# Kernel tuning notes

Measured on AMD Instinct MI355X. Metric: run time of the kernel, lower is better.

## Reference

```python
import jax, jax.numpy as jnp
import numpy as np

N = 100000   # nodes
E = 3200000  # edges
M = 4096     # moves
K = 16       # orders per move
NEG_SLOPE = 0.2  # PyG GATv2Conv default negative_slope

PARAM_SHAPES = {
    'g1_Wl': (10, 15), 'g1_Wr': (10, 15), 'g1_att': (10,), 'g1_b': (10,),
    'g2_Wl': (10, 25), 'g2_Wr': (10, 25), 'g2_att': (10,), 'g2_b': (10,),
    'g3_Wl': (10, 25), 'g3_Wr': (10, 25), 'g3_att': (10,), 'g3_b': (10,),
    'vt_W': (20, 29), 'vt_b': (20,), 'va_W': (1, 20), 'va_b': (1,),
    'vv_W': (10, 20), 'vv_b': (10,), 'vl_W': (1, 10), 'vl_b': (1,),
    'at_W': (20, 48), 'at_b': (20,), 'dt_W': (20, 23), 'dt_b': (20,),
    'oa_W': (1, 20), 'oa_b': (1,), 'ov_W': (1, 20), 'ov_b': (1,),
}
PARAM_NAMES = list(PARAM_SHAPES.keys())


def _linear(x, W, b):
    return x @ W.T + b


def _gatv2(x, src, dst, Wl, Wr, att, b):
    # GATv2Conv (heads=1, self-loops appended by caller), eval mode (no dropout)
    xl = x @ Wl.T  # messages from source nodes
    xr = x @ Wr.T
    e = (jax.nn.leaky_relu(xl[src] + xr[dst], NEG_SLOPE) * att).sum(-1)  # [E+N]
    emax = jax.ops.segment_max(e, dst, num_segments=N)
    ee = jnp.exp(e - emax[dst])
    denom = jax.ops.segment_sum(ee, dst, num_segments=N)
    alpha = ee / denom[dst]
    return jax.ops.segment_sum(alpha[:, None] * xl[src], dst, num_segments=N) + b


def _forward(x1, x2, edges, move_src, move_dst, move_armies, is_attack, params):
    (g1_Wl, g1_Wr, g1_att, g1_b,
     g2_Wl, g2_Wr, g2_att, g2_b,
     g3_Wl, g3_Wr, g3_att, g3_b,
     vt_W, vt_b, va_W, va_b, vv_W, vv_b, vl_W, vl_b,
     at_W, at_b, dt_W, dt_b, oa_W, oa_b, ov_W, ov_b) = params
    x2t = jnp.tile(x2, (N, 1))  # [N,4]
    self_idx = jnp.arange(N, dtype=edges.dtype)
    src = jnp.concatenate([edges[0], self_idx])
    dst = jnp.concatenate([edges[1], self_idx])
    x = jax.nn.relu(_gatv2(x1, src, dst, g1_Wl, g1_Wr, g1_att, g1_b))
    x = jax.nn.relu(_gatv2(jnp.concatenate([x, x1], 1), src, dst, g2_Wl, g2_Wr, g2_att, g2_b))
    x = jax.nn.relu(_gatv2(jnp.concatenate([x, x1], 1), src, dst, g3_Wl, g3_Wr, g3_att, g3_b))  # [N,10]
    # per-move order tensors (vectorized over [M,K]); deploy uses move_src as target
    xs, xd = x[move_src], x[move_dst]       # [M,K,10]
    x1s, x1d = x1[move_src], x1[move_dst]   # [M,K,15]
    extra = 0.6 * move_armies - 0.7 * (x1d[..., 3] + x1d[..., 4])
    attack_in = jnp.concatenate([xs, xd, x1s[..., 3:], x1d[..., 1:],
                                 move_armies[..., None], extra[..., None]], -1)  # [M,K,48]
    deploy_in = jnp.concatenate([xs, x1s[..., 3:], move_armies[..., None]], -1)  # [M,K,23]
    feat = jnp.where(is_attack[..., None] == 1,
                     _linear(attack_in, at_W, at_b),
                     _linear(deploy_in, dt_W, dt_b))
    feat = jax.nn.relu(feat)  # dropout = identity (eval)
    attn = jax.nn.softmax(_linear(feat, oa_W, oa_b), axis=1)  # softmax over orders
    p = (attn * _linear(feat, ov_W, ov_b)).sum(axis=(1, 2))   # [M]
    # value head: attention pooling over all nodes
    Vn = jax.nn.relu(_linear(jnp.concatenate([x, x1, x2t], 1), vt_W, vt_b))  # [N,20]
    vatt = jax.nn.softmax(_linear(Vn, va_W, va_b), axis=0)
    Vp = jax.nn.relu((vatt * _linear(Vn, vv_W, vv_b)).sum(axis=0))
    V = jnp.tanh(_linear(Vp, vl_W, vl_b))[0]
    return V, jax.nn.log_softmax(p, axis=0)


def setup_inputs() -> dict:
    key = jax.random.key(0)
    ks = iter(jax.random.split(key, 64))
    inp = {
        'x1': jax.random.normal(next(ks), (N, 15), jnp.float32),
        'x2': jax.random.normal(next(ks), (4,), jnp.float32),
        'edges': jax.random.randint(next(ks), (2, E), 0, N, jnp.int32),
        'move_src': jax.random.randint(next(ks), (M, K), 0, N, jnp.int32),
        'move_dst': jax.random.randint(next(ks), (M, K), 0, N, jnp.int32),
        'move_armies': jax.random.uniform(next(ks), (M, K), jnp.float32) * 10.0,
        'is_attack': jax.random.randint(next(ks), (M, K), 0, 2, jnp.int32),
    }
    for name, shape in PARAM_SHAPES.items():
        inp[name] = jax.random.normal(next(ks), shape, jnp.float32) * 0.1
    return inp


def reference(x1, x2, edges, move_src, move_dst, move_armies, is_attack,
              g1_Wl, g1_Wr, g1_att, g1_b, g2_Wl, g2_Wr, g2_att, g2_b,
              g3_Wl, g3_Wr, g3_att, g3_b, vt_W, vt_b, va_W, va_b,
              vv_W, vv_b, vl_W, vl_b, at_W, at_b, dt_W, dt_b,
              oa_W, oa_b, ov_W, ov_b):
    params = (g1_Wl, g1_Wr, g1_att, g1_b, g2_Wl, g2_Wr, g2_att, g2_b,
              g3_Wl, g3_Wr, g3_att, g3_b, vt_W, vt_b, va_W, va_b,
              vv_W, vv_b, vl_W, vl_b, at_W, at_b, dt_W, dt_b,
              oa_W, oa_b, ov_W, ov_b)
    return _forward(x1, x2, edges, move_src, move_dst, move_armies, is_attack, params)
```

## Files before the change

kernel.cpp:

```cpp
#include <hip/hip_runtime.h>
#include <hip/hip_bf16.h>
#include <hip/hip_fp16.h>
#include <math.h>

#define NN 100000
#define NE 3200000
#define MM 4096
#define KK 16
#define NEG_SLOPE 0.2f
#define SUB 8
#define BSH 8
#define NB 391
#define PCH 4096
#define FCAP 9728
#define XS 12

__device__ __forceinline__ void load_h10(const __half* __restrict__ base, long node, float* xs) {
    const uint2* p2 = (const uint2*)(base + node * XS);
    uint2 w0 = p2[0];
    uint2 w1 = p2[1];
    unsigned w2 = *(const unsigned*)(base + node * XS + 8);
    float2 f;
    f = __half22float2(*(const __half2*)&w0.x); xs[0] = f.x; xs[1] = f.y;
    f = __half22float2(*(const __half2*)&w0.y); xs[2] = f.x; xs[3] = f.y;
    f = __half22float2(*(const __half2*)&w1.x); xs[4] = f.x; xs[5] = f.y;
    f = __half22float2(*(const __half2*)&w1.y); xs[6] = f.x; xs[7] = f.y;
    f = __half22float2(*(const __half2*)&w2);   xs[8] = f.x; xs[9] = f.y;
}
__device__ __forceinline__ void store_h10(__half* __restrict__ base, long node, const float* v) {
    unsigned u[5];
    #pragma unroll
    for (int q = 0; q < 5; q++) {
        __half2 h = __floats2half2_rn(v[2*q], v[2*q+1]);
        u[q] = *(unsigned*)&h;
    }
    uint2* p2 = (uint2*)(base + node * XS);
    p2[0] = make_uint2(u[0], u[1]);
    p2[1] = make_uint2(u[2], u[3]);
    *(unsigned*)(base + node * XS + 8) = u[4];
}

__global__ __launch_bounds__(512) void partition_kernel(const int* __restrict__ edges,
                                                        int* __restrict__ cnt,
                                                        unsigned* __restrict__ recs) {
    __shared__ unsigned rl[PCH];
    __shared__ unsigned srt[PCH];
    __shared__ unsigned short bb[PCH];
    __shared__ unsigned short bbs[PCH];
    __shared__ int h[NB];
    __shared__ int sc[512];
    __shared__ int lb[NB];
    __shared__ int gb[NB];
    __shared__ int cur[NB];
    const int total = NE + NN;
    int base = blockIdx.x * PCH;
    int n = min(PCH, total - base);
    int t = threadIdx.x;
    for (int i = t; i < NB; i += 512) { h[i] = 0; cur[i] = 0; }
    __syncthreads();
    for (int j = t; j < n; j += 512) {
        int i = base + j;
        int s, d;
        if (i < NE) { s = edges[i]; d = edges[NE + i]; }
        else        { s = i - NE; d = s; }
        rl[j] = ((unsigned)(d & 255) << 17) | (unsigned)s;
        int b = d >> BSH;
        bb[j] = (unsigned short)b;
        atomicAdd(&h[b], 1);
    }
    __syncthreads();
    int hv = (t < NB) ? h[t] : 0;
    sc[t] = hv;
    __syncthreads();
    for (int off = 1; off < 512; off <<= 1) {
        int v = (t >= off) ? sc[t - off] : 0;
        __syncthreads();
        sc[t] += v;
        __syncthreads();
    }
    if (t < NB) {
        lb[t] = sc[t] - hv;
        if (hv > 0) gb[t] = atomicAdd(&cnt[t], hv);
    }
    __syncthreads();
    for (int j = t; j < n; j += 512) {
        int b = bb[j];
        int l = atomicAdd(&cur[b], 1);
        int dst = lb[b] + l;
        srt[dst] = rl[j];
        bbs[dst] = (unsigned short)b;
    }
    __syncthreads();
    for (int j = t; j < n; j += 512) {
        int b = bbs[j];
        int pos = gb[b] + (j - lb[b]);
        if (pos < FCAP) recs[(long)b * FCAP + pos] = srt[j];
    }
}

__global__ void bucket_scan_kernel(const int* __restrict__ cnt, int* __restrict__ bbase) {
    __shared__ int part[512];
    int t = threadIdx.x;
    int c = (t < NB) ? min(cnt[t], FCAP) : 0;
    part[t] = c;
    __syncthreads();
    for (int off = 1; off < 512; off <<= 1) {
        int v = (t >= off) ? part[t - off] : 0;
        __syncthreads();
        part[t] += v;
        __syncthreads();
    }
    if (t < NB) bbase[t] = part[t] - c;
    if (t == NB - 1) bbase[NB] = part[t];
}

__global__ __launch_bounds__(1024) void fine_sort_kernel(const unsigned* __restrict__ recs,
                                                         const int* __restrict__ cnt,
                                                         const int* __restrict__ bbase,
                                                         int* __restrict__ csr_src,
                                                         int* __restrict__ offsets) {
    __shared__ unsigned rl[FCAP];
    __shared__ int hist[256];
    __shared__ int sc[256];
    __shared__ int hb[257];
    __shared__ int cur[256];
    int b = blockIdx.x;
    int beg = bbase[b];
    int nb = min(cnt[b], FCAP);
    int t = threadIdx.x;
    int nodebase = b << BSH;
    int nnodes = min(256, NN - nodebase);
    if (t < 256) { hist[t] = 0; cur[t] = 0; }
    __syncthreads();
    const unsigned* rsrc = recs + (long)b * FCAP;
    for (int j = t; j < nb; j += 1024) {
        unsigned r = rsrc[j];
        rl[j] = r;
        atomicAdd(&hist[r >> 17], 1);
    }
    __syncthreads();
    int hv = (t < 256) ? hist[t] : 0;
    if (t < 256) sc[t] = hv;
    __syncthreads();
    for (int off = 1; off < 256; off <<= 1) {
        int v = 0;
        if (t < 256 && t >= off) v = sc[t - off];
        __syncthreads();
        if (t < 256) sc[t] += v;
        __syncthreads();
    }
    if (t < 256) hb[t] = sc[t] - hv;
    if (t == 0) hb[256] = nb;
    __syncthreads();
    for (int j = t; j < nb; j += 1024) {
        unsigned r = rl[j];
        int l = r >> 17;
        int p = hb[l] + atomicAdd(&cur[l], 1);
        csr_src[beg + p] = (int)(r & 0x1FFFFu);
    }
    if (t < nnodes) offsets[nodebase + t] = beg + hb[t];
    if (b == NB - 1 && t == 0) offsets[NN] = beg + nb;
}

__global__ void linear1_kernel(const float* __restrict__ x1,
                               const float* __restrict__ Wl,
                               const float* __restrict__ Wr,
                               __half* __restrict__ xlh,
                               float* __restrict__ xr) {
    int i = blockIdx.x * blockDim.x + threadIdx.x;
    if (i >= NN) return;
    float in[15];
    #pragma unroll
    for (int j = 0; j < 15; j++) in[j] = x1[i * 15 + j];
    float sl[10];
    #pragma unroll
    for (int o = 0; o < 10; o++) {
        float l = 0.f, r = 0.f;
        #pragma unroll
        for (int j = 0; j < 15; j++) {
            l += Wl[o * 15 + j] * in[j];
            r += Wr[o * 15 + j] * in[j];
        }
        sl[o] = l;
        xr[(long)i * XS + o] = r;
    }
    store_h10(xlh, i, sl);
}

template<bool FUSE_NEXT>
__global__ void gat_aggregate_kernel(const int* __restrict__ csr_src,
                                     const int* __restrict__ offsets,
                                     const __half* __restrict__ xlh,
                                     const float* __restrict__ xr,
                                     const float* __restrict__ att,
                                     const float* __restrict__ b,
                                     const float* __restrict__ x1,
                                     const float* __restrict__ nWl,
                                     const float* __restrict__ nWr,
                                     __half* __restrict__ xlo,
                                     float* __restrict__ xro,
                                     float* __restrict__ xout)
{
    int t = blockIdx.x * blockDim.x + threadIdx.x;
    int node = t / SUB;
    int lane = t % SUB;
    if (node >= NN) return;
    float xrn[12], a[10];
    const float4* xr4 = (const float4*)(xr + (long)node * XS);
    #pragma unroll
    for (int q = 0; q < 3; q++) {
        float4 v = xr4[q];
        xrn[4*q] = v.x; xrn[4*q+1] = v.y; xrn[4*q+2] = v.z; xrn[4*q+3] = v.w;
    }
    #pragma unroll
    for (int h = 0; h < 10; h++) a[h] = att[h];
    int beg = offsets[node], end = offsets[node + 1];
    float den = 0.f, num[10];
    #pragma unroll
    for (int h = 0; h < 10; h++) num[h] = 0.f;
    for (int j = beg + lane; j < end; j += SUB) {
        int s = csr_src[j];
        float xs[10];
        load_h10(xlh, s, xs);
        float e = 0.f;
        #pragma unroll
        for (int h = 0; h < 10; h++) {
            float v = xs[h] + xrn[h];
            v = (v >= 0.f) ? v : NEG_SLOPE * v;
            e += v * a[h];
        }
        float w = __expf(e);
        den += w;
        #pragma unroll
        for (int h = 0; h < 10; h++) num[h] += w * xs[h];
    }
    #pragma unroll
    for (int off = SUB / 2; off; off >>= 1) {
        den += __shfl_xor(den, off, SUB);
        #pragma unroll
        for (int h = 0; h < 10; h++) num[h] += __shfl_xor(num[h], off, SUB);
    }
    float inv = 1.f / den;
    float xo[10];
    #pragma unroll
    for (int h = 0; h < 10; h++) xo[h] = fmaxf(num[h] * inv + b[h], 0.f);
    if (FUSE_NEXT) {
        if (lane < 5) {
            float in2[25];
            #pragma unroll
            for (int h = 0; h < 10; h++) in2[h] = xo[h];
            #pragma unroll
            for (int h = 0; h < 15; h++) in2[10 + h] = x1[(long)node * 15 + h];
            int o0 = 2 * lane, o1 = 2 * lane + 1;
            float sl0 = 0.f, sl1 = 0.f, sr0 = 0.f, sr1 = 0.f;
            #pragma unroll
            for (int j = 0; j < 25; j++) {
                sl0 += nWl[o0 * 25 + j] * in2[j];
                sl1 += nWl[o1 * 25 + j] * in2[j];
                sr0 += nWr[o0 * 25 + j] * in2[j];
                sr1 += nWr[o1 * 25 + j] * in2[j];
            }
            __half2 hp = __floats2half2_rn(sl0, sl1);
            *(unsigned*)(xlo + (long)node * XS + o0) = *(unsigned*)&hp;
            *(float2*)(xro + (long)node * XS + o0) = make_float2(sr0, sr1);
        }
    } else {
        if (lane == 0) {
            #pragma unroll
            for (int h = 0; h < 10; h++) xout[(long)node * XS + h] = xo[h];
        }
    }
}

__global__ void move_kernel(const float* __restrict__ x,
                            const float* __restrict__ x1,
                            const int* __restrict__ msrc,
                            const int* __restrict__ mdst,
                            const float* __restrict__ armies,
                            const int* __restrict__ isatk,
                            const float* __restrict__ at_W, const float* __restrict__ at_b,
                            const float* __restrict__ dt_W, const float* __restrict__ dt_b,
                            const float* __restrict__ oa_W, const float* __restrict__ oa_b,
                            const float* __restrict__ ov_W, const float* __restrict__ ov_b,
                            float* __restrict__ p) {
    int t = blockIdx.x * blockDim.x + threadIdx.x;
    int m = t >> 4;
    int k = t & 15;
    int s = msrc[t], d = mdst[t];
    float arm = armies[t];
    bool atk = (isatk[t] == 1);
    float xsrc[12];
    const float4* xs4 = (const float4*)(x + (long)s * XS);
    #pragma unroll
    for (int q = 0; q < 3; q++) {
        float4 v = xs4[q];
        xsrc[4*q] = v.x; xsrc[4*q+1] = v.y; xsrc[4*q+2] = v.z; xsrc[4*q+3] = v.w;
    }
    float feat[20];
    if (atk) {
        float in[48];
        #pragma unroll
        for (int h = 0; h < 10; h++) in[h] = xsrc[h];
        const float4* xd4 = (const float4*)(x + (long)d * XS);
        float xdst[12];
        #pragma unroll
        for (int q = 0; q < 3; q++) {
            float4 v = xd4[q];
            xdst[4*q] = v.x; xdst[4*q+1] = v.y; xdst[4*q+2] = v.z; xdst[4*q+3] = v.w;
        }
        #pragma unroll
        for (int h = 0; h < 10; h++) in[10 + h] = xdst[h];
        #pragma unroll
        for (int h = 0; h < 12; h++) in[20 + h] = x1[(long)s * 15 + 3 + h];
        #pragma unroll
        for (int h = 0; h < 14; h++) in[32 + h] = x1[(long)d * 15 + 1 + h];
        in[46] = arm;
        in[47] = 0.6f * arm - 0.7f * (x1[(long)d * 15 + 3] + x1[(long)d * 15 + 4]);
        #pragma unroll
        for (int o = 0; o < 20; o++) {
            float sum = at_b[o];
            #pragma unroll
            for (int j = 0; j < 48; j++) sum += at_W[o * 48 + j] * in[j];
            feat[o] = fmaxf(sum, 0.f);
        }
    } else {
        float in[23];
        #pragma unroll
        for (int h = 0; h < 10; h++) in[h] = xsrc[h];
        #pragma unroll
        for (int h = 0; h < 12; h++) in[10 + h] = x1[(long)s * 15 + 3 + h];
        in[22] = arm;
        #pragma unroll
        for (int o = 0; o < 20; o++) {
            float sum = dt_b[o];
            #pragma unroll
            for (int j = 0; j < 23; j++) sum += dt_W[o * 23 + j] * in[j];
            feat[o] = fmaxf(sum, 0.f);
        }
    }
    float oa = oa_b[0], ov = ov_b[0];
    #pragma unroll
    for (int j = 0; j < 20; j++) {
        oa += oa_W[j] * feat[j];
        ov += ov_W[j] * feat[j];
    }
    float mx = oa;
    #pragma unroll
    for (int off = 8; off; off >>= 1) mx = fmaxf(mx, __shfl_xor(mx, off, 16));
    float w = __expf(oa - mx);
    float nume = w * ov;
    float den = w;
    #pragma unroll
    for (int off = 8; off; off >>= 1) {
        nume += __shfl_xor(nume, off, 16);
        den  += __shfl_xor(den,  off, 16);
    }
    if (k == 0) p[m] = nume / den;
}

__global__ void logsoftmax_kernel(const float* __restrict__ p, float* __restrict__ out) {
    __shared__ float sm[256];
    int tid = threadIdx.x;
    float mx = -INFINITY;
    for (int i = tid; i < MM; i += 256) mx = fmaxf(mx, p[i]);
    sm[tid] = mx; __syncthreads();
    for (int s = 128; s; s >>= 1) { if (tid < s) sm[tid] = fmaxf(sm[tid], sm[tid + s]); __syncthreads(); }
    mx = sm[0]; __syncthreads();
    float sum = 0.f;
    for (int i = tid; i < MM; i += 256) sum += expf(p[i] - mx);
    sm[tid] = sum; __syncthreads();
    for (int s = 128; s; s >>= 1) { if (tid < s) sm[tid] += sm[tid + s]; __syncthreads(); }
    float ls = mx + logf(sm[0]);
    for (int i = tid; i < MM; i += 256) out[i] = p[i] - ls;
}

__global__ void value12_kernel(const float* __restrict__ x,
                               const float* __restrict__ x1,
                               const float* __restrict__ x2,
                               const float* __restrict__ vt_W, const float* __restrict__ vt_b,
                               const float* __restrict__ va_W, const float* __restrict__ va_b,
                               const float* __restrict__ vv_W, const float* __restrict__ vv_b,
                               float* __restrict__ partials) {
    __shared__ float sm[4][11];
    int i = blockIdx.x * blockDim.x + threadIdx.x;
    float w = 0.f;
    float acc[10];
    #pragma unroll
    for (int h = 0; h < 10; h++) acc[h] = 0.f;
    if (i < NN) {
        float in[29];
        const float4* xi4 = (const float4*)(x + (long)i * XS);
        float xi[12];
        #pragma unroll
        for (int q = 0; q < 3; q++) {
            float4 v = xi4[q];
            xi[4*q] = v.x; xi[4*q+1] = v.y; xi[4*q+2] = v.z; xi[4*q+3] = v.w;
        }
        #pragma unroll
        for (int h = 0; h < 10; h++) in[h] = xi[h];
        #pragma unroll
        for (int h = 0; h < 15; h++) in[10 + h] = x1[(long)i * 15 + h];
        #pragma unroll
        for (int h = 0; h < 4; h++) in[25 + h] = x2[h];
        float Vn[20];
        #pragma unroll
        for (int o = 0; o < 20; o++) {
            float s = vt_b[o];
            #pragma unroll
            for (int j = 0; j < 29; j++) s += vt_W[o * 29 + j] * in[j];
            Vn[o] = fmaxf(s, 0.f);
        }
        float lg = va_b[0];
        #pragma unroll
        for (int j = 0; j < 20; j++) lg += va_W[j] * Vn[j];
        w = __expf(lg);
        #pragma unroll
        for (int o = 0; o < 10; o++) {
            float s = vv_b[o];
            #pragma unroll
            for (int j = 0; j < 20; j++) s += vv_W[o * 20 + j] * Vn[j];
            acc[o] = w * s;
        }
    }
    #pragma unroll
    for (int off = 32; off; off >>= 1) {
        w += __shfl_xor(w, off, 64);
        #pragma unroll
        for (int h = 0; h < 10; h++) acc[h] += __shfl_xor(acc[h], off, 64);
    }
    int wid = threadIdx.x >> 6;
    if ((threadIdx.x & 63) == 0) {
        #pragma unroll
        for (int h = 0; h < 10; h++) sm[wid][h] = acc[h];
        sm[wid][10] = w;
    }
    __syncthreads();
    if (threadIdx.x < 11) {
        int c = threadIdx.x;
        partials[(long)blockIdx.x * 12 + c] = sm[0][c] + sm[1][c] + sm[2][c] + sm[3][c];
    }
}

__global__ void value3_kernel(const float* __restrict__ partials, int nparts,
                              const float* __restrict__ vl_W, const float* __restrict__ vl_b,
                              float* __restrict__ out0) {
    int lane = threadIdx.x;
    float s[11];
    #pragma unroll
    for (int c = 0; c < 11; c++) s[c] = 0.f;
    for (int j = lane; j < nparts; j += 64)
        #pragma unroll
        for (int c = 0; c < 11; c++) s[c] += partials[(long)j * 12 + c];
    #pragma unroll
    for (int off = 32; off; off >>= 1)
        #pragma unroll
        for (int c = 0; c < 11; c++) s[c] += __shfl_xor(s[c], off, 64);
    if (lane == 0) {
        float inv = 1.0f / s[10];
        float v = vl_b[0];
        #pragma unroll
        for (int h = 0; h < 10; h++) v += vl_W[h] * fmaxf(s[h] * inv, 0.f);
        out0[0] = tanhf(v);
    }
}

extern "C" void kernel_launch(void* const* d_in, const int* in_sizes, int n_in,
                              void* d_out, int out_size, void* d_ws, size_t ws_size,
                              hipStream_t stream) {
    const float* x1      = (const float*)d_in[0];
    const float* x2      = (const float*)d_in[1];
    const int*   edges   = (const int*)d_in[2];
    const int*   msrc    = (const int*)d_in[3];
    const int*   mdst    = (const int*)d_in[4];
    const float* armies  = (const float*)d_in[5];
    const int*   isatk   = (const int*)d_in[6];
    const float* g1_Wl = (const float*)d_in[7],  *g1_Wr = (const float*)d_in[8];
    const float* g1_att= (const float*)d_in[9],  *g1_b  = (const float*)d_in[10];
    const float* g2_Wl = (const float*)d_in[11], *g2_Wr = (const float*)d_in[12];
    const float* g2_att= (const float*)d_in[13], *g2_b  = (const float*)d_in[14];
    const float* g3_Wl = (const float*)d_in[15], *g3_Wr = (const float*)d_in[16];
    const float* g3_att= (const float*)d_in[17], *g3_b  = (const float*)d_in[18];
    const float* vt_W  = (const float*)d_in[19], *vt_b  = (const float*)d_in[20];
    const float* va_W  = (const float*)d_in[21], *va_b  = (const float*)d_in[22];
    const float* vv_W  = (const float*)d_in[23], *vv_b  = (const float*)d_in[24];
    const float* vl_W  = (const float*)d_in[25], *vl_b  = (const float*)d_in[26];
    const float* at_W  = (const float*)d_in[27], *at_b  = (const float*)d_in[28];
    const float* dt_W  = (const float*)d_in[29], *dt_b  = (const float*)d_in[30];
    const float* oa_W  = (const float*)d_in[31], *oa_b  = (const float*)d_in[32];
    const float* ov_W  = (const float*)d_in[33], *ov_b  = (const float*)d_in[34];

    float* out = (float*)d_out;

    float* ws = (float*)d_ws;
    const long XN = (long)NN * XS;
    __half* xlhA = (__half*)ws;
    __half* xlhB = xlhA + XN;
    float* xrA = (float*)(xlhB + XN);
    float* xrB = xrA + XN;
    float* xF  = xrB + XN;
    int* csr_src = (int*)(xF + XN);
    int* offsets = csr_src + (NE + NN);
    unsigned* recs = (unsigned*)(offsets + NN + 4);
    int* cnt   = (int*)(recs + (long)NB * FCAP);
    int* bbase = cnt + NB + 1;
    float* pbuf = (float*)(bbase + NB + 3);
    float* partials = pbuf + MM;

    const int nodeBlocks = (NN + 255) / 256;
    const int aggBlocks  = ((long)NN * SUB + 255) / 256;
    const int partBlocks = (NE + NN + PCH - 1) / PCH;

    hipMemsetAsync(cnt, 0, NB * sizeof(int), stream);
    partition_kernel<<<partBlocks, 512, 0, stream>>>(edges, cnt, recs);
    bucket_scan_kernel<<<1, 512, 0, stream>>>(cnt, bbase);
    fine_sort_kernel<<<NB, 1024, 0, stream>>>(recs, cnt, bbase, csr_src, offsets);

    linear1_kernel<<<nodeBlocks, 256, 0, stream>>>(x1, g1_Wl, g1_Wr, xlhA, xrA);
    gat_aggregate_kernel<true><<<aggBlocks, 256, 0, stream>>>(
        csr_src, offsets, xlhA, xrA, g1_att, g1_b, x1, g2_Wl, g2_Wr, xlhB, xrB, nullptr);
    gat_aggregate_kernel<true><<<aggBlocks, 256, 0, stream>>>(
        csr_src, offsets, xlhB, xrB, g2_att, g2_b, x1, g3_Wl, g3_Wr, xlhA, xrA, nullptr);
    gat_aggregate_kernel<false><<<aggBlocks, 256, 0, stream>>>(
        csr_src, offsets, xlhA, xrA, g3_att, g3_b, x1, nullptr, nullptr, nullptr, nullptr, xF);

    move_kernel<<<(MM * KK) / 256, 256, 0, stream>>>(
        xF, x1, msrc, mdst, armies, isatk,
        at_W, at_b, dt_W, dt_b, oa_W, oa_b, ov_W, ov_b, pbuf);
    logsoftmax_kernel<<<1, 256, 0, stream>>>(pbuf, out + 1);

    value12_kernel<<<nodeBlocks, 256, 0, stream>>>(
        xF, x1, x2, vt_W, vt_b, va_W, va_b, vv_W, vv_b, partials);
    value3_kernel<<<1, 64, 0, stream>>>(partials, nodeBlocks, vl_W, vl_b, out);
}
```

Before: 366.9 us.

## Aggregate directly from coarse bucket records with shared-memory atomics, drop fine sort

Removes the bucket scan and fine CSR sort kernels. Each GAT aggregation block now processes one 256-node destination bucket straight from the partitioned records, accumulating numerators and denominators with shared-memory float atomics. The next layer's linear projection runs from shared weights. The fp16 feature rows are padded to 16 halves so one 16-byte load fetches most of a row, and the partition kernel uses 1024 threads. This saves the sort passes and CSR writes at the cost of heavy shared-atomic contention and only 391 blocks per layer, which may leave the GPU underoccupied.

```diff
diff --git a/kernel.cpp b/kernel.cpp
--- a/kernel.cpp
+++ b/kernel.cpp
@@ -8,47 +8,22 @@
 #define MM 4096
 #define KK 16
 #define NEG_SLOPE 0.2f
-#define SUB 8
 #define BSH 8
 #define NB 391
 #define PCH 4096
 #define FCAP 9728
 #define XS 12
-
-__device__ __forceinline__ void load_h10(const __half* __restrict__ base, long node, float* xs) {
-    const uint2* p2 = (const uint2*)(base + node * XS);
-    uint2 w0 = p2[0];
-    uint2 w1 = p2[1];
-    unsigned w2 = *(const unsigned*)(base + node * XS + 8);
-    float2 f;
-    f = __half22float2(*(const __half2*)&w0.x); xs[0] = f.x; xs[1] = f.y;
-    f = __half22float2(*(const __half2*)&w0.y); xs[2] = f.x; xs[3] = f.y;
-    f = __half22float2(*(const __half2*)&w1.x); xs[4] = f.x; xs[5] = f.y;
-    f = __half22float2(*(const __half2*)&w1.y); xs[6] = f.x; xs[7] = f.y;
-    f = __half22float2(*(const __half2*)&w2);   xs[8] = f.x; xs[9] = f.y;
-}
-__device__ __forceinline__ void store_h10(__half* __restrict__ base, long node, const float* v) {
-    unsigned u[5];
-    #pragma unroll
-    for (int q = 0; q < 5; q++) {
-        __half2 h = __floats2half2_rn(v[2*q], v[2*q+1]);
-        u[q] = *(unsigned*)&h;
-    }
-    uint2* p2 = (uint2*)(base + node * XS);
-    p2[0] = make_uint2(u[0], u[1]);
-    p2[1] = make_uint2(u[2], u[3]);
-    *(unsigned*)(base + node * XS + 8) = u[4];
-}
-
-__global__ __launch_bounds__(512) void partition_kernel(const int* __restrict__ edges,
-                                                        int* __restrict__ cnt,
-                                                        unsigned* __restrict__ recs) {
+#define XSH 16
+
+__global__ __launch_bounds__(1024) void partition_kernel(const int* __restrict__ edges,
+                                                         int* __restrict__ cnt,
+                                                         unsigned* __restrict__ recs) {
     __shared__ unsigned rl[PCH];
     __shared__ unsigned srt[PCH];
     __shared__ unsigned short bb[PCH];
     __shared__ unsigned short bbs[PCH];
     __shared__ int h[NB];
-    __shared__ int sc[512];
+    __shared__ int sc[1024];
     __shared__ int lb[NB];
     __shared__ int gb[NB];
     __shared__ int cur[NB];
@@ -56,9 +31,9 @@
     int base = blockIdx.x * PCH;
     int n = min(PCH, total - base);
     int t = threadIdx.x;
-    for (int i = t; i < NB; i += 512) { h[i] = 0; cur[i] = 0; }
-    __syncthreads();
-    for (int j = t; j < n; j += 512) {
+    if (t < NB) { h[t] = 0; cur[t] = 0; }
+    __syncthreads();
+    for (int j = t; j < n; j += 1024) {
         int i = base + j;
         int s, d;
         if (i < NE) { s = edges[i]; d = edges[NE + i]; }
@@ -72,7 +47,7 @@
     int hv = (t < NB) ? h[t] : 0;
     sc[t] = hv;
     __syncthreads();
-    for (int off = 1; off < 512; off <<= 1) {
+    for (int off = 1; off < 1024; off <<= 1) {
         int v = (t >= off) ? sc[t - off] : 0;
         __syncthreads();
         sc[t] += v;
@@ -83,7 +58,7 @@
         if (hv > 0) gb[t] = atomicAdd(&cnt[t], hv);
     }
     __syncthreads();
-    for (int j = t; j < n; j += 512) {
+    for (int j = t; j < n; j += 1024) {
         int b = bb[j];
         int l = atomicAdd(&cur[b], 1);
         int dst = lb[b] + l;
@@ -91,75 +66,11 @@
         bbs[dst] = (unsigned short)b;
     }
     __syncthreads();
-    for (int j = t; j < n; j += 512) {
+    for (int j = t; j < n; j += 1024) {
         int b = bbs[j];
         int pos = gb[b] + (j - lb[b]);
         if (pos < FCAP) recs[(long)b * FCAP + pos] = srt[j];
     }
-}
-
-__global__ void bucket_scan_kernel(const int* __restrict__ cnt, int* __restrict__ bbase) {
-    __shared__ int part[512];
-    int t = threadIdx.x;
-    int c = (t < NB) ? min(cnt[t], FCAP) : 0;
-    part[t] = c;
-    __syncthreads();
-    for (int off = 1; off < 512; off <<= 1) {
-        int v = (t >= off) ? part[t - off] : 0;
-        __syncthreads();
-        part[t] += v;
-        __syncthreads();
-    }
-    if (t < NB) bbase[t] = part[t] - c;
-    if (t == NB - 1) bbase[NB] = part[t];
-}
-
-__global__ __launch_bounds__(1024) void fine_sort_kernel(const unsigned* __restrict__ recs,
-                                                         const int* __restrict__ cnt,
-                                                         const int* __restrict__ bbase,
-                                                         int* __restrict__ csr_src,
-                                                         int* __restrict__ offsets) {
-    __shared__ unsigned rl[FCAP];
-    __shared__ int hist[256];
-    __shared__ int sc[256];
-    __shared__ int hb[257];
-    __shared__ int cur[256];
-    int b = blockIdx.x;
-    int beg = bbase[b];
-    int nb = min(cnt[b], FCAP);
-    int t = threadIdx.x;
-    int nodebase = b << BSH;
-    int nnodes = min(256, NN - nodebase);
-    if (t < 256) { hist[t] = 0; cur[t] = 0; }
-    __syncthreads();
-    const unsigned* rsrc = recs + (long)b * FCAP;
-    for (int j = t; j < nb; j += 1024) {
-        unsigned r = rsrc[j];
-        rl[j] = r;
-        atomicAdd(&hist[r >> 17], 1);
-    }
-    __syncthreads();
-    int hv = (t < 256) ? hist[t] : 0;
-    if (t < 256) sc[t] = hv;
-    __syncthreads();
-    for (int off = 1; off < 256; off <<= 1) {
-        int v = 0;
-        if (t < 256 && t >= off) v = sc[t - off];
-        __syncthreads();
-        if (t < 256) sc[t] += v;
-        __syncthreads();
-    }
-    if (t < 256) hb[t] = sc[t] - hv;
-    if (t == 0) hb[256] = nb;
-    __syncthreads();
-    for (int j = t; j < nb; j += 1024) {
-        unsigned r = rl[j];
-        int l = r >> 17;
-        int p = hb[l] + atomicAdd(&cur[l], 1);
-        csr_src[beg + p] = (int)(r & 0x1FFFFu);
-    }
-    if (t < nnodes) offsets[nodebase + t] = beg + hb[t];
-    if (b == NB - 1 && t == 0) offsets[NN] = beg + nb;
 }
 
 __global__ void linear1_kernel(const float* __restrict__ x1,
@@ -184,44 +95,72 @@
         sl[o] = l;
         xr[(long)i * XS + o] = r;
     }
-    store_h10(xlh, i, sl);
+    unsigned u[5];
+    #pragma unroll
+    for (int q = 0; q < 5; q++) {
+        __half2 hh = __floats2half2_rn(sl[2*q], sl[2*q+1]);
+        u[q] = *(unsigned*)&hh;
+    }
+    uint4* p4 = (uint4*)(xlh + (long)i * XSH);
+    p4[0] = make_uint4(u[0], u[1], u[2], u[3]);
+    *(unsigned*)(xlh + (long)i * XSH + 8) = u[4];
 }
 
 template<bool FUSE_NEXT>
-__global__ void gat_aggregate_kernel(const int* __restrict__ csr_src,
-                                     const int* __restrict__ offsets,
-                                     const __half* __restrict__ xlh,
-                                     const float* __restrict__ xr,
-                                     const float* __restrict__ att,
-                                     const float* __restrict__ b,
-                                     const float* __restrict__ x1,
-                                     const float* __restrict__ nWl,
-                                     const float* __restrict__ nWr,
-                                     __half* __restrict__ xlo,
-                                     float* __restrict__ xro,
-                                     float* __restrict__ xout)
+__global__ __launch_bounds__(1024) void rec_aggregate_kernel(
+        const unsigned* __restrict__ recs,
+        const int* __restrict__ cnt,
+        const __half* __restrict__ xlh,
+        const float* __restrict__ xr,
+        const float* __restrict__ att,
+        const float* __restrict__ bias,
+        const float* __restrict__ x1,
+        const float* __restrict__ nWl,
+        const float* __restrict__ nWr,
+        __half* __restrict__ xlo,
+        float* __restrict__ xro,
+        float* __restrict__ xout)
 {
-    int t = blockIdx.x * blockDim.x + threadIdx.x;
-    int node = t / SUB;
-    int lane = t % SUB;
-    if (node >= NN) return;
-    float xrn[12], a[10];
-    const float4* xr4 = (const float4*)(xr + (long)node * XS);
-    #pragma unroll
-    for (int q = 0; q < 3; q++) {
-        float4 v = xr4[q];
-        xrn[4*q] = v.x; xrn[4*q+1] = v.y; xrn[4*q+2] = v.z; xrn[4*q+3] = v.w;
-    }
+    __shared__ float xrt[256 * 11];
+    __shared__ float acc[256 * 11];
+    __shared__ float wsh[500];
+    int b = blockIdx.x;
+    int t = threadIdx.x;
+    int nodebase = b << BSH;
+    int nnodes = min(256, NN - nodebase);
+    int nb = min(cnt[b], FCAP);
+    if (t < nnodes) {
+        const float* p = xr + (long)(nodebase + t) * XS;
+        float4 a0 = *(const float4*)p;
+        float4 a1 = *(const float4*)(p + 4);
+        float2 a2 = *(const float2*)(p + 8);
+        float* dst = xrt + t * 11;
+        dst[0]=a0.x; dst[1]=a0.y; dst[2]=a0.z; dst[3]=a0.w;
+        dst[4]=a1.x; dst[5]=a1.y; dst[6]=a1.z; dst[7]=a1.w;
+        dst[8]=a2.x; dst[9]=a2.y;
+    }
+    for (int i = t; i < 256 * 11; i += 1024) acc[i] = 0.f;
+    if (FUSE_NEXT && t < 500) wsh[t] = (t < 250) ? nWl[t] : nWr[t - 250];
+    float a[10];
     #pragma unroll
     for (int h = 0; h < 10; h++) a[h] = att[h];
-    int beg = offsets[node], end = offsets[node + 1];
-    float den = 0.f, num[10];
-    #pragma unroll
-    for (int h = 0; h < 10; h++) num[h] = 0.f;
-    for (int j = beg + lane; j < end; j += SUB) {
-        int s = csr_src[j];
+    __syncthreads();
+    const unsigned* rsrc = recs + (long)b * FCAP;
+    for (int j = t; j < nb; j += 1024) {
+        unsigned r = rsrc[j];
+        int dl = r >> 17;
+        int s = r & 0x1FFFFu;
+        const __half* ph = xlh + (long)s * XSH;
+        uint4 w0 = *(const uint4*)ph;
+        uint2 w1 = *(const uint2*)(ph + 8);
         float xs[10];
-        load_h10(xlh, s, xs);
+        float2 f;
+        f = __half22float2(*(const __half2*)&w0.x); xs[0]=f.x; xs[1]=f.y;
+        f = __half22float2(*(const __half2*)&w0.y); xs[2]=f.x; xs[3]=f.y;
+        f = __half22float2(*(const __half2*)&w0.z); xs[4]=f.x; xs[5]=f.y;
+        f = __half22float2(*(const __half2*)&w0.w); xs[6]=f.x; xs[7]=f.y;
+        f = __half22float2(*(const __half2*)&w1.x); xs[8]=f.x; xs[9]=f.y;
+        const float* xrn = xrt + dl * 11;
         float e = 0.f;
         #pragma unroll
         for (int h = 0; h < 10; h++) {
@@ -230,44 +169,56 @@
             e += v * a[h];
         }
         float w = __expf(e);
-        den += w;
-        #pragma unroll
-        for (int h = 0; h < 10; h++) num[h] += w * xs[h];
-    }
-    #pragma unroll
-    for (int off = SUB / 2; off; off >>= 1) {
-        den += __shfl_xor(den, off, SUB);
-        #pragma unroll
-        for (int h = 0; h < 10; h++) num[h] += __shfl_xor(num[h], off, SUB);
-    }
-    float inv = 1.f / den;
-    float xo[10];
-    #pragma unroll
-    for (int h = 0; h < 10; h++) xo[h] = fmaxf(num[h] * inv + b[h], 0.f);
+        float* pa = acc + dl * 11;
+        #pragma unroll
+        for (int h = 0; h < 10; h++) atomicAdd(&pa[h], w * xs[h]);
+        atomicAdd(&pa[10], w);
+    }
+    __syncthreads();
+    if (t < nnodes) {
+        float* pa = acc + t * 11;
+        float inv = 1.f / pa[10];
+        #pragma unroll
+        for (int h = 0; h < 10; h++)
+            pa[h] = fmaxf(pa[h] * inv + bias[h], 0.f);
+    }
+    __syncthreads();
     if (FUSE_NEXT) {
-        if (lane < 5) {
+        int node = t >> 2;
+        int sub = t & 3;
+        if (node < nnodes) {
             float in2[25];
-            #pragma unroll
-            for (int h = 0; h < 10; h++) in2[h] = xo[h];
-            #pragma unroll
-            for (int h = 0; h < 15; h++) in2[10 + h] = x1[(long)node * 15 + h];
-            int o0 = 2 * lane, o1 = 2 * lane + 1;
-            float sl0 = 0.f, sl1 = 0.f, sr0 = 0.f, sr1 = 0.f;
-            #pragma unroll
-            for (int j = 0; j < 25; j++) {
-                sl0 += nWl[o0 * 25 + j] * in2[j];
-                sl1 += nWl[o1 * 25 + j] * in2[j];
-                sr0 += nWr[o0 * 25 + j] * in2[j];
-                sr1 += nWr[o1 * 25 + j] * in2[j];
+            const float* pa = acc + node * 11;
+            #pragma unroll
+            for (int h = 0; h < 10; h++) in2[h] = pa[h];
+            const float* px1 = x1 + (long)(nodebase + node) * 15;
+            #pragma unroll
+            for (int h = 0; h < 15; h++) in2[10 + h] = px1[h];
+            #pragma unroll
+            for (int rep = 0; rep < 2; rep++) {
+                int p = sub + rep * 4;
+                if (p < 5) {
+                    int o0 = 2 * p, o1 = 2 * p + 1;
+                    float sl0 = 0.f, sl1 = 0.f, sr0 = 0.f, sr1 = 0.f;
+                    #pragma unroll
+                    for (int j = 0; j < 25; j++) {
+                        sl0 += wsh[o0 * 25 + j] * in2[j];
+                        sl1 += wsh[o1 * 25 + j] * in2[j];
+                        sr0 += wsh[250 + o0 * 25 + j] * in2[j];
+                        sr1 += wsh[250 + o1 * 25 + j] * in2[j];
+                    }
+                    __half2 hp = __floats2half2_rn(sl0, sl1);
+                    *(unsigned*)(xlo + (long)(nodebase + node) * XSH + o0) = *(unsigned*)&hp;
+                    *(float2*)(xro + (long)(nodebase + node) * XS + o0) = make_float2(sr0, sr1);
+                }
             }
-            __half2 hp = __floats2half2_rn(sl0, sl1);
-            *(unsigned*)(xlo + (long)node * XS + o0) = *(unsigned*)&hp;
-            *(float2*)(xro + (long)node * XS + o0) = make_float2(sr0, sr1);
         }
     } else {
-        if (lane == 0) {
-            #pragma unroll
-            for (int h = 0; h < 10; h++) xout[(long)node * XS + h] = xo[h];
+        if (t < nnodes) {
+            const float* pa = acc + t * 11;
+            float* po = xout + (long)(nodebase + t) * XS;
+            #pragma unroll
+            for (int h = 0; h < 10; h++) po[h] = pa[h];
         }
     }
 }
@@ -492,36 +443,29 @@
     float* out = (float*)d_out;
 
     float* ws = (float*)d_ws;
-    const long XN = (long)NN * XS;
     __half* xlhA = (__half*)ws;
-    __half* xlhB = xlhA + XN;
-    float* xrA = (float*)(xlhB + XN);
-    float* xrB = xrA + XN;
-    float* xF  = xrB + XN;
-    int* csr_src = (int*)(xF + XN);
-    int* offsets = csr_src + (NE + NN);
-    unsigned* recs = (unsigned*)(offsets + NN + 4);
+    __half* xlhB = xlhA + (long)NN * XSH;
+    float* xrA = (float*)(xlhB + (long)NN * XSH);
+    float* xrB = xrA + (long)NN * XS;
+    float* xF  = xrB + (long)NN * XS;
+    unsigned* recs = (unsigned*)(xF + (long)NN * XS);
     int* cnt   = (int*)(recs + (long)NB * FCAP);
-    int* bbase = cnt + NB + 1;
-    float* pbuf = (float*)(bbase + NB + 3);
+    float* pbuf = (float*)(cnt + NB + 1);
     float* partials = pbuf + MM;
 
     const int nodeBlocks = (NN + 255) / 256;
-    const int aggBlocks  = ((long)NN * SUB + 255) / 256;
     const int partBlocks = (NE + NN + PCH - 1) / PCH;
 
     hipMemsetAsync(cnt, 0, NB * sizeof(int), stream);
-    partition_kernel<<<partBlocks, 512, 0, stream>>>(edges, cnt, recs);
-    bucket_scan_kernel<<<1, 512, 0, stream>>>(cnt, bbase);
-    fine_sort_kernel<<<NB, 1024, 0, stream>>>(recs, cnt, bbase, csr_src, offsets);
+    partition_kernel<<<partBlocks, 1024, 0, stream>>>(edges, cnt, recs);
 
     linear1_kernel<<<nodeBlocks, 256, 0, stream>>>(x1, g1_Wl, g1_Wr, xlhA, xrA);
-    gat_aggregate_kernel<true><<<aggBlocks, 256, 0, stream>>>(
-        csr_src, offsets, xlhA, xrA, g1_att, g1_b, x1, g2_Wl, g2_Wr, xlhB, xrB, nullptr);
-    gat_aggregate_kernel<true><<<aggBlocks, 256, 0, stream>>>(
-        csr_src, offsets, xlhB, xrB, g2_att, g2_b, x1, g3_Wl, g3_Wr, xlhA, xrA, nullptr);
-    gat_aggregate_kernel<false><<<aggBlocks, 256, 0, stream>>>(
-        csr_src, offsets, xlhA, xrA, g3_att, g3_b, x1, nullptr, nullptr, nullptr, nullptr, xF);
+    rec_aggregate_kernel<true><<<NB, 1024, 0, stream>>>(
+        recs, cnt, xlhA, xrA, g1_att, g1_b, x1, g2_Wl, g2_Wr, xlhB, xrB, nullptr);
+    rec_aggregate_kernel<true><<<NB, 1024, 0, stream>>>(
+        recs, cnt, xlhB, xrB, g2_att, g2_b, x1, g3_Wl, g3_Wr, xlhA, xrA, nullptr);
+    rec_aggregate_kernel<false><<<NB, 1024, 0, stream>>>(
+        recs, cnt, xlhA, xrA, g3_att, g3_b, x1, nullptr, nullptr, nullptr, nullptr, xF);
 
     move_kernel<<<(MM * KK) / 256, 256, 0, stream>>>(
         xF, x1, msrc, mdst, armies, isatk,
```

After: 997.7 us. +171.9%, slower.

## Pad fp16 node features to 32 bytes, unroll edge gathers, widen partition blocks

Applied to the files above, without the earlier changes.

Source-feature rows in half precision go from a 24-byte stride to a 32-byte stride, so each gathered row is one aligned 16-byte load plus one 4-byte load that no longer straddles cache sectors. The aggregation loop is unrolled four ways, issuing four independent index and feature gathers before computing, to hide memory latency. The partition kernel also moves from 512 to 1024 threads per block. The padding uses more workspace and memory footprint, and the larger unroll raises register pressure, which may lower occupancy.

```diff
diff --git a/kernel.cpp b/kernel.cpp
--- a/kernel.cpp
+++ b/kernel.cpp
@@ -14,41 +14,26 @@
 #define PCH 4096
 #define FCAP 9728
 #define XS 12
-
-__device__ __forceinline__ void load_h10(const __half* __restrict__ base, long node, float* xs) {
-    const uint2* p2 = (const uint2*)(base + node * XS);
-    uint2 w0 = p2[0];
-    uint2 w1 = p2[1];
-    unsigned w2 = *(const unsigned*)(base + node * XS + 8);
+#define XSH 16
+
+__device__ __forceinline__ void h10_to_f(const uint4& w0, unsigned w2, float* xs) {
     float2 f;
-    f = __half22float2(*(const __half2*)&w0.x); xs[0] = f.x; xs[1] = f.y;
-    f = __half22float2(*(const __half2*)&w0.y); xs[2] = f.x; xs[3] = f.y;
-    f = __half22float2(*(const __half2*)&w1.x); xs[4] = f.x; xs[5] = f.y;
-    f = __half22float2(*(const __half2*)&w1.y); xs[6] = f.x; xs[7] = f.y;
-    f = __half22float2(*(const __half2*)&w2);   xs[8] = f.x; xs[9] = f.y;
-}
-__device__ __forceinline__ void store_h10(__half* __restrict__ base, long node, const float* v) {
-    unsigned u[5];
-    #pragma unroll
-    for (int q = 0; q < 5; q++) {
-        __half2 h = __floats2half2_rn(v[2*q], v[2*q+1]);
-        u[q] = *(unsigned*)&h;
-    }
-    uint2* p2 = (uint2*)(base + node * XS);
-    p2[0] = make_uint2(u[0], u[1]);
-    p2[1] = make_uint2(u[2], u[3]);
-    *(unsigned*)(base + node * XS + 8) = u[4];
-}
-
-__global__ __launch_bounds__(512) void partition_kernel(const int* __restrict__ edges,
-                                                        int* __restrict__ cnt,
-                                                        unsigned* __restrict__ recs) {
+    f = __half22float2(*(const __half2*)&w0.x); xs[0]=f.x; xs[1]=f.y;
+    f = __half22float2(*(const __half2*)&w0.y); xs[2]=f.x; xs[3]=f.y;
+    f = __half22float2(*(const __half2*)&w0.z); xs[4]=f.x; xs[5]=f.y;
+    f = __half22float2(*(const __half2*)&w0.w); xs[6]=f.x; xs[7]=f.y;
+    f = __half22float2(*(const __half2*)&w2);   xs[8]=f.x; xs[9]=f.y;
+}
+
+__global__ __launch_bounds__(1024) void partition_kernel(const int* __restrict__ edges,
+                                                         int* __restrict__ cnt,
+                                                         unsigned* __restrict__ recs) {
     __shared__ unsigned rl[PCH];
     __shared__ unsigned srt[PCH];
     __shared__ unsigned short bb[PCH];
     __shared__ unsigned short bbs[PCH];
     __shared__ int h[NB];
-    __shared__ int sc[512];
+    __shared__ int sc[1024];
     __shared__ int lb[NB];
     __shared__ int gb[NB];
     __shared__ int cur[NB];
@@ -56,9 +41,9 @@
     int base = blockIdx.x * PCH;
     int n = min(PCH, total - base);
     int t = threadIdx.x;
-    for (int i = t; i < NB; i += 512) { h[i] = 0; cur[i] = 0; }
-    __syncthreads();
-    for (int j = t; j < n; j += 512) {
+    if (t < NB) { h[t] = 0; cur[t] = 0; }
+    __syncthreads();
+    for (int j = t; j < n; j += 1024) {
         int i = base + j;
         int s, d;
         if (i < NE) { s = edges[i]; d = edges[NE + i]; }
@@ -72,7 +57,7 @@
     int hv = (t < NB) ? h[t] : 0;
     sc[t] = hv;
     __syncthreads();
-    for (int off = 1; off < 512; off <<= 1) {
+    for (int off = 1; off < 1024; off <<= 1) {
         int v = (t >= off) ? sc[t - off] : 0;
         __syncthreads();
         sc[t] += v;
@@ -83,7 +68,7 @@
         if (hv > 0) gb[t] = atomicAdd(&cnt[t], hv);
     }
     __syncthreads();
-    for (int j = t; j < n; j += 512) {
+    for (int j = t; j < n; j += 1024) {
         int b = bb[j];
         int l = atomicAdd(&cur[b], 1);
         int dst = lb[b] + l;
@@ -91,7 +76,7 @@
         bbs[dst] = (unsigned short)b;
     }
     __syncthreads();
-    for (int j = t; j < n; j += 512) {
+    for (int j = t; j < n; j += 1024) {
         int b = bbs[j];
         int pos = gb[b] + (j - lb[b]);
         if (pos < FCAP) recs[(long)b * FCAP + pos] = srt[j];
@@ -184,7 +169,15 @@
         sl[o] = l;
         xr[(long)i * XS + o] = r;
     }
-    store_h10(xlh, i, sl);
+    unsigned u[5];
+    #pragma unroll
+    for (int q = 0; q < 5; q++) {
+        __half2 hh = __floats2half2_rn(sl[2*q], sl[2*q+1]);
+        u[q] = *(unsigned*)&hh;
+    }
+    uint4* p4 = (uint4*)(xlh + (long)i * XSH);
+    p4[0] = make_uint4(u[0], u[1], u[2], u[3]);
+    *(uint2*)(xlh + (long)i * XSH + 8) = make_uint2(u[4], 0u);
 }
 
 template<bool FUSE_NEXT>
@@ -218,10 +211,44 @@
     float den = 0.f, num[10];
     #pragma unroll
     for (int h = 0; h < 10; h++) num[h] = 0.f;
-    for (int j = beg + lane; j < end; j += SUB) {
+    int j = beg + lane;
+    for (; j + 3 * SUB < end; j += 4 * SUB) {
+        int s0 = csr_src[j];
+        int s1 = csr_src[j + SUB];
+        int s2 = csr_src[j + 2 * SUB];
+        int s3 = csr_src[j + 3 * SUB];
+        const __half *p0 = xlh + (long)s0 * XSH, *p1 = xlh + (long)s1 * XSH;
+        const __half *p2 = xlh + (long)s2 * XSH, *p3 = xlh + (long)s3 * XSH;
+        uint4 w0a = *(const uint4*)p0; unsigned w0b = *(const unsigned*)(p0 + 8);
+        uint4 w1a = *(const uint4*)p1; unsigned w1b = *(const unsigned*)(p1 + 8);
+        uint4 w2a = *(const uint4*)p2; unsigned w2b = *(const unsigned*)(p2 + 8);
+        uint4 w3a = *(const uint4*)p3; unsigned w3b = *(const unsigned*)(p3 + 8);
+        uint4 wa[4] = {w0a, w1a, w2a, w3a};
+        unsigned wb[4] = {w0b, w1b, w2b, w3b};
+        #pragma unroll
+        for (int q = 0; q < 4; q++) {
+            float xs[10];
+            h10_to_f(wa[q], wb[q], xs);
+            float e = 0.f;
+            #pragma unroll
+            for (int h = 0; h < 10; h++) {
+                float v = xs[h] + xrn[h];
+                v = (v >= 0.f) ? v : NEG_SLOPE * v;
+                e += v * a[h];
+            }
+            float w = __expf(e);
+            den += w;
+            #pragma unroll
+            for (int h = 0; h < 10; h++) num[h] += w * xs[h];
+        }
+    }
+    for (; j < end; j += SUB) {
         int s = csr_src[j];
+        const __half* ph = xlh + (long)s * XSH;
+        uint4 wa = *(const uint4*)ph;
+        unsigned wb = *(const unsigned*)(ph + 8);
         float xs[10];
-        load_h10(xlh, s, xs);
+        h10_to_f(wa, wb, xs);
         float e = 0.f;
         #pragma unroll
         for (int h = 0; h < 10; h++) {
@@ -254,14 +281,14 @@
             int o0 = 2 * lane, o1 = 2 * lane + 1;
             float sl0 = 0.f, sl1 = 0.f, sr0 = 0.f, sr1 = 0.f;
             #pragma unroll
-            for (int j = 0; j < 25; j++) {
-                sl0 += nWl[o0 * 25 + j] * in2[j];
-                sl1 += nWl[o1 * 25 + j] * in2[j];
-                sr0 += nWr[o0 * 25 + j] * in2[j];
-                sr1 += nWr[o1 * 25 + j] * in2[j];
+            for (int jj = 0; jj < 25; jj++) {
+                sl0 += nWl[o0 * 25 + jj] * in2[jj];
+                sl1 += nWl[o1 * 25 + jj] * in2[jj];
+                sr0 += nWr[o0 * 25 + jj] * in2[jj];
+                sr1 += nWr[o1 * 25 + jj] * in2[jj];
             }
             __half2 hp = __floats2half2_rn(sl0, sl1);
-            *(unsigned*)(xlo + (long)node * XS + o0) = *(unsigned*)&hp;
+            *(unsigned*)(xlo + (long)node * XSH + o0) = *(unsigned*)&hp;
             *(float2*)(xro + (long)node * XS + o0) = make_float2(sr0, sr1);
         }
     } else {
@@ -492,13 +519,12 @@
     float* out = (float*)d_out;
 
     float* ws = (float*)d_ws;
-    const long XN = (long)NN * XS;
     __half* xlhA = (__half*)ws;
-    __half* xlhB = xlhA + XN;
-    float* xrA = (float*)(xlhB + XN);
-    float* xrB = xrA + XN;
-    float* xF  = xrB + XN;
-    int* csr_src = (int*)(xF + XN);
+    __half* xlhB = xlhA + (long)NN * XSH;
+    float* xrA = (float*)(xlhB + (long)NN * XSH);
+    float* xrB = xrA + (long)NN * XS;
+    float* xF  = xrB + (long)NN * XS;
+    int* csr_src = (int*)(xF + (long)NN * XS);
     int* offsets = csr_src + (NE + NN);
     unsigned* recs = (unsigned*)(offsets + NN + 4);
     int* cnt   = (int*)(recs + (long)NB * FCAP);
@@ -511,7 +537,7 @@
     const int partBlocks = (NE + NN + PCH - 1) / PCH;
 
     hipMemsetAsync(cnt, 0, NB * sizeof(int), stream);
-    partition_kernel<<<partBlocks, 512, 0, stream>>>(edges, cnt, recs);
+    partition_kernel<<<partBlocks, 1024, 0, stream>>>(edges, cnt, recs);
     bucket_scan_kernel<<<1, 512, 0, stream>>>(cnt, bbase);
     fine_sort_kernel<<<NB, 1024, 0, stream>>>(recs, cnt, bbase, csr_src, offsets);
 
```

After: 377.7 us. 2.9% more time.
